# Optimization experiments

Measured on AMD Instinct MI355X. Metric: run time of the kernel, lower is better.

## Reference

```python
import jax, jax.numpy as jnp
import numpy as np


def setup_inputs() -> dict:
    key = jax.random.key(0)
    ks = jax.random.split(key, 16)
    B, T, A, R, M, D = 128, 1024, 512, 1024, 256, 256  # batch, max_time, annot, rnn, memory, attn dims
    F, K = 32, 31  # location filters, kernel size
    s = jnp.float32(0.02)
    return dict(
        memory=jax.random.normal(ks[0], (B, M), jnp.float32),
        context=jax.random.normal(ks[1], (B, A), jnp.float32),
        rnn_state=jax.random.normal(ks[2], (B, R), jnp.float32),
        annots=jax.random.normal(ks[3], (B, T, A), jnp.float32),
        atten=jax.random.uniform(ks[4], (B, 2, T), jnp.float32),
        mask=jax.random.randint(ks[5], (B, T), 0, 2).astype(jnp.int32),
        Wi=jax.random.normal(ks[6], (3 * R, A + M), jnp.float32) * s,   # GRU input weights (r,z,n)
        Wh=jax.random.normal(ks[7], (3 * R, R), jnp.float32) * s,       # GRU hidden weights
        bi=jnp.zeros((3 * R,), jnp.float32),
        bh=jnp.zeros((3 * R,), jnp.float32),
        conv_w=jax.random.normal(ks[8], (F, 2, K), jnp.float32) * s,    # loc_conv (OIH)
        loc_w=jax.random.normal(ks[9], (D, F), jnp.float32) * s,
        loc_b=jnp.zeros((D,), jnp.float32),
        q_w=jax.random.normal(ks[10], (D, R), jnp.float32) * s,
        q_b=jnp.zeros((D,), jnp.float32),
        a_w=jax.random.normal(ks[11], (D, A), jnp.float32) * s,
        a_b=jnp.zeros((D,), jnp.float32),
        v_w=jax.random.normal(ks[12], (1, D), jnp.float32) * s,
    )


def reference(memory, context, rnn_state, annots, atten, mask,
              Wi, Wh, bi, bh, conv_w, loc_w, loc_b, q_w, q_b, a_w, a_b, v_w):
    # --- GRUCell (torch gate order: r, z, n) ---
    x = jnp.concatenate([memory, context], axis=-1)          # (B, M+A)
    gi = x @ Wi.T + bi                                        # (B, 3R)
    gh = rnn_state @ Wh.T + bh                                # (B, 3R)
    ir, iz, inn = jnp.split(gi, 3, axis=-1)
    hr, hz, hn = jnp.split(gh, 3, axis=-1)
    r = jax.nn.sigmoid(ir + hr)
    z = jax.nn.sigmoid(iz + hz)
    n = jnp.tanh(inn + r * hn)
    h = (1.0 - z) * n + z * rnn_state                         # (B, R) rnn_output

    # --- Location-sensitive attention ---
    pad = (conv_w.shape[-1] - 1) // 2
    loc = jax.lax.conv_general_dilated(atten, conv_w, (1,), [(pad, pad)],
                                       dimension_numbers=('NCH', 'OIH', 'NCH'))  # (B, F, T)
    ploc = jnp.einsum('bft,df->btd', loc, loc_w) + loc_b      # (B, T, D)
    pq = (h @ q_w.T + q_b)[:, None, :]                        # (B, 1, D)
    pa = jnp.einsum('bta,da->btd', annots, a_w) + a_b         # (B, T, D)
    align = jnp.einsum('btd,d->bt', jnp.tanh(pq + pa + ploc), v_w[0])  # (B, T)

    # masked softmax (mask==0 -> -inf)
    align = jnp.where(mask != 0, align, jnp.float32(-1e30))
    align = jax.nn.softmax(align, axis=-1)

    # context = bmm(align, annots)
    ctx = jnp.einsum('bt,bta->ba', align, annots)             # (B, A)
    return (h, ctx, align)
```

## Files before the change

kernel.cpp:

```cpp
#include <hip/hip_runtime.h>
#include <cstddef>

constexpr int B  = 128;
constexpr int T  = 1024;
constexpr int AD = 512;
constexpr int R  = 1024;
constexpr int M  = 256;
constexpr int DD = 256;
constexpr int F  = 32;
constexpr int KW = 31;
constexpr int PADW = 15;
constexpr int XDIM = M + AD;
constexpr int G3 = 3 * R;
constexpr size_t BG3 = (size_t)B * G3;

using short8 = __attribute__((ext_vector_type(8))) short;
using f32x4  = __attribute__((ext_vector_type(4))) float;

__device__ __forceinline__ float sigmoidf(float x) { return 1.f / (1.f + __expf(-x)); }

__device__ __forceinline__ unsigned short f2bf(float x) {
  unsigned int u = __float_as_uint(x);
  u += 0x7FFFu + ((u >> 16) & 1u);
  return (unsigned short)(u >> 16);
}

__device__ __forceinline__ float tanh_fast(float x) {
  float e = __expf(2.f * x);
  return 1.f - 2.f / (e + 1.f);
}

__device__ __forceinline__ void load_lds16(const void* g, void* l) {
  __builtin_amdgcn_global_load_lds(
      (const __attribute__((address_space(1))) unsigned int*)g,
      (__attribute__((address_space(3))) unsigned int*)l, 16, 0, 0);
}

__global__ __launch_bounds__(256) void prep_wsw(const float* __restrict__ aw,
                                                const float* __restrict__ lw,
                                                unsigned short* __restrict__ awsw,
                                                unsigned short* __restrict__ lwsw) {
  int idx = blockIdx.x * 256 + threadIdx.x;
  int chunk = idx >> 10;
  int rn = (idx & 1023) >> 2;
  int u = idx & 3;
  int su = u ^ ((rn >> 1) & 3);
  const float* src;
  unsigned short* dst;
  if (chunk < 16) {
    src = aw + (size_t)rn * AD + chunk * 32 + u * 8;
    dst = awsw + chunk * 8192 + rn * 32 + su * 8;
  } else {
    src = lw + (size_t)rn * F + u * 8;
    dst = lwsw + rn * 32 + su * 8;
  }
  float4 f0 = *(const float4*)src;
  float4 f1 = *(const float4*)(src + 4);
  unsigned int w0 = f2bf(f0.x) | ((unsigned)f2bf(f0.y) << 16);
  unsigned int w1 = f2bf(f0.z) | ((unsigned)f2bf(f0.w) << 16);
  unsigned int w2 = f2bf(f1.x) | ((unsigned)f2bf(f1.y) << 16);
  unsigned int w3 = f2bf(f1.z) | ((unsigned)f2bf(f1.w) << 16);
  uint4 pk = {w0, w1, w2, w3};
  *(uint4*)dst = pk;
}

__global__ __launch_bounds__(256) void loc_conv(const float* __restrict__ atten,
                                                const float* __restrict__ conv_w,
                                                unsigned short* __restrict__ locw) {
  __shared__ float s_att[2 * 94];
  __shared__ float s_cw[F * 62];
  const int tid = threadIdx.x;
  const int t0 = blockIdx.x * 64, b = blockIdx.y;
  for (int i = tid; i < 2 * 94; i += 256) {
    int c = i / 94, ii = i - c * 94;
    int gt = t0 - PADW + ii;
    s_att[i] = (gt >= 0 && gt < T) ? atten[((size_t)b * 2 + c) * T + gt] : 0.f;
  }
  for (int i = tid; i < F * 62; i += 256) s_cw[i] = conv_w[i];
  __syncthreads();
  const int f = tid & 31;
  const int tb = (tid >> 5) * 8;
  float a8[8] = {0.f, 0.f, 0.f, 0.f, 0.f, 0.f, 0.f, 0.f};
#pragma unroll
  for (int c = 0; c < 2; ++c) {
    float win[38];
#pragma unroll
    for (int i = 0; i < 38; ++i) win[i] = s_att[c * 94 + tb + i];
#pragma unroll
    for (int k = 0; k < KW; ++k) {
      float w = s_cw[f * 62 + c * 31 + k];
#pragma unroll
      for (int ti = 0; ti < 8; ++ti) a8[ti] += w * win[ti + k];
    }
  }
#pragma unroll
  for (int ti = 0; ti < 8; ++ti)
    locw[((size_t)b * T + t0 + tb + ti) * F + f] = f2bf(a8[ti]);
}

__global__ __launch_bounds__(256) void gemm_fused8(const float* __restrict__ mem,
                                                   const float* __restrict__ ctxin,
                                                   const float* __restrict__ rnn,
                                                   const float* __restrict__ Wi,
                                                   const float* __restrict__ Wh,
                                                   float* __restrict__ outp) {
  __shared__ __align__(16) float sX[16 * 68];
  __shared__ __align__(16) float sW[16 * 68];
  const int z = blockIdx.z;
  const int which = z >> 2, q = z & 3;
  const float* __restrict__ W = which ? Wh : Wi;
  const int K = which ? R : XDIM;
  const int Kq = K >> 2;
  const int kbeg = q * Kq, kend = kbeg + Kq;
  float* __restrict__ C = outp + (size_t)z * BG3;
  const int tid = threadIdx.x;
  const int g0 = blockIdx.x * 64, b0 = blockIdx.y * 64;
  const int bg = tid & 15, gg = tid >> 4;
  const int lr = tid >> 2, c4 = (tid & 3) * 4;
  float acc[4][4] = {};
  for (int k0 = kbeg; k0 < kend; k0 += 16) {
    const int k = k0 + c4;
    float4 xv;
    if (which) xv = *(const float4*)&rnn[(size_t)(b0 + lr) * R + k];
    else if (k < M) xv = *(const float4*)&mem[(size_t)(b0 + lr) * M + k];
    else xv = *(const float4*)&ctxin[(size_t)(b0 + lr) * AD + (k - M)];
    float4 wv = *(const float4*)&W[(size_t)(g0 + lr) * K + k];
    sX[(c4 + 0) * 68 + lr] = xv.x; sX[(c4 + 1) * 68 + lr] = xv.y;
    sX[(c4 + 2) * 68 + lr] = xv.z; sX[(c4 + 3) * 68 + lr] = xv.w;
    sW[(c4 + 0) * 68 + lr] = wv.x; sW[(c4 + 1) * 68 + lr] = wv.y;
    sW[(c4 + 2) * 68 + lr] = wv.z; sW[(c4 + 3) * 68 + lr] = wv.w;
    __syncthreads();
#pragma unroll
    for (int k2 = 0; k2 < 16; ++k2) {
      float4 xr = *(const float4*)&sX[k2 * 68 + bg * 4];
      float4 wr = *(const float4*)&sW[k2 * 68 + gg * 4];
      float xa[4] = {xr.x, xr.y, xr.z, xr.w};
      float wa[4] = {wr.x, wr.y, wr.z, wr.w};
#pragma unroll
      for (int ib = 0; ib < 4; ++ib)
#pragma unroll
        for (int jg = 0; jg < 4; ++jg) acc[ib][jg] += xa[ib] * wa[jg];
    }
    __syncthreads();
  }
#pragma unroll
  for (int ib = 0; ib < 4; ++ib) {
    float4 o;
    o.x = acc[ib][0]; o.y = acc[ib][1]; o.z = acc[ib][2]; o.w = acc[ib][3];
    *(float4*)&C[(size_t)(b0 + bg * 4 + ib) * G3 + g0 + gg * 4] = o;
  }
}

__global__ __launch_bounds__(256) void gru_combine(const float* __restrict__ gp,
                                                   const float* __restrict__ bi,
                                                   const float* __restrict__ bh,
                                                   const float* __restrict__ hprev,
                                                   float* __restrict__ hout) {
  int idx = blockIdx.x * 256 + threadIdx.x;
  int b = idx >> 10, j = idx & (R - 1);
  float ir = bi[j], iz = bi[R + j], inn = bi[2 * R + j];
  float hr = bh[j], hz = bh[R + j], hn = bh[2 * R + j];
#pragma unroll
  for (int z = 0; z < 4; ++z) {
    const float* g = gp + (size_t)z * BG3 + (size_t)b * G3;
    ir += g[j]; iz += g[R + j]; inn += g[2 * R + j];
  }
#pragma unroll
  for (int z = 4; z < 8; ++z) {
    const float* g = gp + (size_t)z * BG3 + (size_t)b * G3;
    hr += g[j]; hz += g[R + j]; hn += g[2 * R + j];
  }
  float r = sigmoidf(ir + hr);
  float z = sigmoidf(iz + hz);
  float n = tanhf(inn + r * hn);
  float hp = hprev[(size_t)b * R + j];
  hout[(size_t)b * R + j] = (1.f - z) * n + z * hp;
}

__global__ __launch_bounds__(256) void pq_kernel(const float* __restrict__ h,
                                                 const float* __restrict__ q_w,
                                                 const float* __restrict__ q_b,
                                                 float* __restrict__ pq) {
  __shared__ __align__(16) float sh[R];
  int b = blockIdx.x, tid = threadIdx.x;
  ((float4*)sh)[tid] = ((const float4*)(h + (size_t)b * R))[tid];
  __syncthreads();
  const float* wr = q_w + (size_t)tid * R;
  float acc = 0.f;
#pragma unroll 4
  for (int k = 0; k < R; k += 4) {
    float4 w = *(const float4*)&wr[k];
    float4 x = *(const float4*)&sh[k];
    acc += w.x * x.x + w.y * x.y + w.z * x.z + w.w * x.w;
  }
  pq[(size_t)b * DD + tid] = acc + q_b[tid];
}

__global__ __launch_bounds__(512, 4) void attn_fused(
    const float* __restrict__ annots, const unsigned short* __restrict__ locw,
    const int* __restrict__ mask,
    const unsigned short* __restrict__ awsw, const unsigned short* __restrict__ lwsw,
    const float* __restrict__ loc_b, const float* __restrict__ a_b,
    const float* __restrict__ v_w, const float* __restrict__ pq,
    float* __restrict__ u_out, float* __restrict__ ctx_part,
    float* __restrict__ S_part) {
  __shared__ __align__(16) unsigned short s_A[2][128 * 32];
  __shared__ __align__(16) unsigned short s_B[2][256 * 32];

  const int tid = threadIdx.x;
  const int wv = tid >> 6, lane = tid & 63;
  const int lm = lane & 15, lg = lane >> 4;
  const int wr = wv >> 2, wc = wv & 3;
  const int g = blockIdx.x, b = blockIdx.y;
  const int t0 = g * 128;
  const int ar = tid >> 2, au = tid & 3;
  const int asu = au ^ ((ar >> 1) & 3);
  const int sufb = lg ^ ((lm >> 1) & 3);

  const float* arow = annots + ((size_t)b * T + t0 + ar) * AD + au * 8;

  {
    float4 f0 = *(const float4*)(arow);
    float4 f1 = *(const float4*)(arow + 4);
    load_lds16(awsw + wv * 1024 + lane * 8, &s_B[0][wv * 1024]);
    load_lds16(awsw + wv * 1024 + 512 + lane * 8, &s_B[0][wv * 1024 + 512]);
    unsigned int w0 = f2bf(f0.x) | ((unsigned)f2bf(f0.y) << 16);
    unsigned int w1 = f2bf(f0.z) | ((unsigned)f2bf(f0.w) << 16);
    unsigned int w2 = f2bf(f1.x) | ((unsigned)f2bf(f1.y) << 16);
    unsigned int w3 = f2bf(f1.z) | ((unsigned)f2bf(f1.w) << 16);
    uint4 pk = {w0, w1, w2, w3};
    *(uint4*)&s_A[0][ar * 32 + asu * 8] = pk;
  }
  float4 aN0 = *(const float4*)(arow + 32);
  float4 aN1 = *(const float4*)(arow + 36);
  uint4 lvN = {0, 0, 0, 0};

  f32x4 acc[4][4];
#pragma unroll
  for (int j = 0; j < 4; ++j) {
    int d = wc * 64 + j * 16 + lm;
    float base = pq[(size_t)b * DD + d] + a_b[d] + loc_b[d];
    f32x4 bv = {base, base, base, base};
#pragma unroll
    for (int i = 0; i < 4; ++i) acc[i][j] = bv;
  }
  __syncthreads();

#pragma unroll 1
  for (int ks = 0; ks <= 16; ++ks) {
    const int cur = ks & 1, nxt = cur ^ 1;
    if (ks + 1 <= 16) {
      const unsigned short* img = (ks + 1 < 16) ? (awsw + (ks + 1) * 8192) : lwsw;
      load_lds16(img + wv * 1024 + lane * 8, &s_B[nxt][wv * 1024]);
      load_lds16(img + wv * 1024 + 512 + lane * 8, &s_B[nxt][wv * 1024 + 512]);
    }
    float4 aN20, aN21;
    uint4 lvN2;
    if (ks + 2 <= 15) {
      aN20 = *(const float4*)(arow + (ks + 2) * 32);
      aN21 = *(const float4*)(arow + (ks + 2) * 32 + 4);
    } else if (ks + 2 == 16) {
      lvN2 = *(const uint4*)(locw + ((size_t)b * T + t0 + ar) * F + au * 8);
    }
    if (ks + 1 <= 15) {
      unsigned int w0 = f2bf(aN0.x) | ((unsigned)f2bf(aN0.y) << 16);
      unsigned int w1 = f2bf(aN0.z) | ((unsigned)f2bf(aN0.w) << 16);
      unsigned int w2 = f2bf(aN1.x) | ((unsigned)f2bf(aN1.y) << 16);
      unsigned int w3 = f2bf(aN1.z) | ((unsigned)f2bf(aN1.w) << 16);
      uint4 pk = {w0, w1, w2, w3};
      *(uint4*)&s_A[nxt][ar * 32 + asu * 8] = pk;
    } else if (ks + 1 == 16) {
      *(uint4*)&s_A[nxt][ar * 32 + asu * 8] = lvN;
    }
    short8 afr[4], bfr[4];
#pragma unroll
    for (int i = 0; i < 4; ++i)
      afr[i] = *(const short8*)&s_A[cur][(wr * 64 + i * 16 + lm) * 32 + sufb * 8];
#pragma unroll
    for (int j = 0; j < 4; ++j)
      bfr[j] = *(const short8*)&s_B[cur][(wc * 64 + j * 16 + lm) * 32 + sufb * 8];
#pragma unroll
    for (int j = 0; j < 4; ++j)
#pragma unroll
      for (int i = 0; i < 4; ++i)
        acc[i][j] = __builtin_amdgcn_mfma_f32_16x16x32_bf16(afr[i], bfr[j], acc[i][j], 0, 0, 0);
    if (ks <= 13) {
      asm volatile("s_waitcnt vmcnt(2) lgkmcnt(0)" ::: "memory");
    } else if (ks == 14) {
      asm volatile("s_waitcnt vmcnt(1) lgkmcnt(0)" ::: "memory");
    } else {
      asm volatile("s_waitcnt vmcnt(0) lgkmcnt(0)" ::: "memory");
    }
    __builtin_amdgcn_s_barrier();
    if (ks + 2 <= 15) { aN0 = aN20; aN1 = aN21; }
    else if (ks + 2 == 16) lvN = lvN2;
  }

  float* s_e = (float*)s_A;
  float* s_u = s_e + 512;
  float* s_red = s_e + 644;
  float vwv[4];
#pragma unroll
  for (int j = 0; j < 4; ++j) vwv[j] = v_w[wc * 64 + j * 16 + lm];
#pragma unroll
  for (int i = 0; i < 4; ++i) {
#pragma unroll
    for (int reg = 0; reg < 4; ++reg) {
      float p = 0.f;
#pragma unroll
      for (int j = 0; j < 4; ++j) p += vwv[j] * tanh_fast(acc[i][j][reg]);
      p += __shfl_xor(p, 1);
      p += __shfl_xor(p, 2);
      p += __shfl_xor(p, 4);
      p += __shfl_xor(p, 8);
      if (lm == 0) s_e[wc * 128 + wr * 64 + i * 16 + lg * 4 + reg] = p;
    }
  }
  __syncthreads();
  if (tid < 128) {
    float e = s_e[tid] + s_e[128 + tid] + s_e[256 + tid] + s_e[384 + tid];
    bool mk = mask[(size_t)b * T + t0 + tid] != 0;
    float u = mk ? __expf(e) : 0.f;
    u_out[(size_t)b * T + t0 + tid] = u;
    s_u[tid] = u;
    float p = u;
    p += __shfl_xor(p, 1);
    p += __shfl_xor(p, 2);
    p += __shfl_xor(p, 4);
    p += __shfl_xor(p, 8);
    p += __shfl_xor(p, 16);
    p += __shfl_xor(p, 32);
    if (lane == 0) s_red[tid >> 6] = p;
  }
  __syncthreads();
  if (tid == 0) S_part[b * 8 + g] = s_red[0] + s_red[1];
  {
    const float* ap = annots + ((size_t)b * T + t0) * AD + tid;
    float c0 = 0.f, c1 = 0.f, c2 = 0.f, c3 = 0.f;
#pragma unroll 2
    for (int t = 0; t < 128; t += 4) {
      c0 += s_u[t + 0] * ap[(size_t)(t + 0) * AD];
      c1 += s_u[t + 1] * ap[(size_t)(t + 1) * AD];
      c2 += s_u[t + 2] * ap[(size_t)(t + 2) * AD];
      c3 += s_u[t + 3] * ap[(size_t)(t + 3) * AD];
    }
    ctx_part[(size_t)g * ((size_t)B * AD) + (size_t)b * AD + tid] = (c0 + c1) + (c2 + c3);
  }
}

__global__ __launch_bounds__(512) void finalize(const float* __restrict__ S_part,
                                                const float* __restrict__ ctx_part,
                                                float* __restrict__ al,
                                                float* __restrict__ ctxo) {
  int b = blockIdx.x, tid = threadIdx.x;
  float S = 0.f;
#pragma unroll
  for (int g = 0; g < 8; ++g) S += S_part[b * 8 + g];
  float inv = 1.f / S;
  float2* ap = (float2*)(al + (size_t)b * T);
  float2 v = ap[tid];
  v.x *= inv; v.y *= inv;
  ap[tid] = v;
  float c = 0.f;
#pragma unroll
  for (int p = 0; p < 8; ++p)
    c += ctx_part[(size_t)p * ((size_t)B * AD) + (size_t)b * AD + tid];
  ctxo[(size_t)b * AD + tid] = c * inv;
}

extern "C" void kernel_launch(void* const* d_in, const int* in_sizes, int n_in,
                              void* d_out, int out_size, void* d_ws, size_t ws_size,
                              hipStream_t stream) {
  const float* memory = (const float*)d_in[0];
  const float* context = (const float*)d_in[1];
  const float* rnn = (const float*)d_in[2];
  const float* annots = (const float*)d_in[3];
  const float* atten = (const float*)d_in[4];
  const int* mask = (const int*)d_in[5];
  const float* Wi = (const float*)d_in[6];
  const float* Wh = (const float*)d_in[7];
  const float* bi = (const float*)d_in[8];
  const float* bh = (const float*)d_in[9];
  const float* conv_w = (const float*)d_in[10];
  const float* loc_w = (const float*)d_in[11];
  const float* loc_b = (const float*)d_in[12];
  const float* q_w = (const float*)d_in[13];
  const float* q_b = (const float*)d_in[14];
  const float* a_w = (const float*)d_in[15];
  const float* a_b = (const float*)d_in[16];
  const float* v_w = (const float*)d_in[17];

  float* out = (float*)d_out;
  float* out_h = out;
  float* out_ctx = out + (size_t)B * R;
  float* out_al = out_ctx + (size_t)B * AD;

  float* ws = (float*)d_ws;
  float* gp_ws = ws;
  float* pq_ws = gp_ws + 8 * BG3;
  float* S_part = pq_ws + (size_t)B * DD;
  float* ctx_part = S_part + (size_t)B * 8;
  unsigned short* awsw = (unsigned short*)(ctx_part + (size_t)8 * B * AD);
  unsigned short* lwsw = awsw + (size_t)16 * 8192;
  unsigned short* locws = lwsw + 8192;

  prep_wsw<<<68, 256, 0, stream>>>(a_w, loc_w, awsw, lwsw);
  loc_conv<<<dim3(T / 64, B), 256, 0, stream>>>(atten, conv_w, locws);
  gemm_fused8<<<dim3(G3 / 64, B / 64, 8), 256, 0, stream>>>(memory, context, rnn,
                                                            Wi, Wh, gp_ws);
  gru_combine<<<(B * R) / 256, 256, 0, stream>>>(gp_ws, bi, bh, rnn, out_h);
  pq_kernel<<<B, 256, 0, stream>>>(out_h, q_w, q_b, pq_ws);
  attn_fused<<<dim3(8, B), 512, 0, stream>>>(annots, locws, mask, awsw, lwsw,
                                             loc_b, a_b, v_w, pq_ws,
                                             out_al, ctx_part, S_part);
  finalize<<<B, 512, 0, stream>>>(S_part, ctx_part, out_al, out_ctx);
}
```

Before: 190.2 us.

## Convert GRU GEMM inputs to bf16 and compute gates with MFMA

Adds a prep kernel that converts Wi, Wh, the concatenated input and the hidden state to bf16 in workspace. The fp32 LDS-tiled FMA GEMM is replaced by an MFMA 16x16x32 bf16 kernel that reads fragments straight from global memory, with no LDS staging, still split-K into 8 partials. The aim is to swap slow scalar FP32 FMAs for matrix cores. In exchange it adds a full pass over the weights every call (fp32 read plus bf16 write), uses bf16 precision for the GRU, and the direct global fragment loads are not coalesced.

```diff
diff --git a/kernel.cpp b/kernel.cpp
--- a/kernel.cpp
+++ b/kernel.cpp
@@ -28,6 +28,15 @@
 __device__ __forceinline__ float tanh_fast(float x) {
   float e = __expf(2.f * x);
   return 1.f - 2.f / (e + 1.f);
+}
+
+__device__ __forceinline__ uint4 pack_bf8(float4 f0, float4 f1) {
+  uint4 r;
+  r.x = f2bf(f0.x) | ((unsigned)f2bf(f0.y) << 16);
+  r.y = f2bf(f0.z) | ((unsigned)f2bf(f0.w) << 16);
+  r.z = f2bf(f1.x) | ((unsigned)f2bf(f1.y) << 16);
+  r.w = f2bf(f1.z) | ((unsigned)f2bf(f1.w) << 16);
+  return r;
 }
 
 __device__ __forceinline__ void load_lds16(const void* g, void* l) {
@@ -56,12 +65,42 @@
   }
   float4 f0 = *(const float4*)src;
   float4 f1 = *(const float4*)(src + 4);
-  unsigned int w0 = f2bf(f0.x) | ((unsigned)f2bf(f0.y) << 16);
-  unsigned int w1 = f2bf(f0.z) | ((unsigned)f2bf(f0.w) << 16);
-  unsigned int w2 = f2bf(f1.x) | ((unsigned)f2bf(f1.y) << 16);
-  unsigned int w3 = f2bf(f1.z) | ((unsigned)f2bf(f1.w) << 16);
-  uint4 pk = {w0, w1, w2, w3};
-  *(uint4*)dst = pk;
+  *(uint4*)dst = pack_bf8(f0, f1);
+}
+
+__global__ __launch_bounds__(256) void prep_gru(const float* __restrict__ mem,
+                                                const float* __restrict__ ctxin,
+                                                const float* __restrict__ rnn,
+                                                const float* __restrict__ Wi,
+                                                const float* __restrict__ Wh,
+                                                unsigned short* __restrict__ Wib,
+                                                unsigned short* __restrict__ Whb,
+                                                unsigned short* __restrict__ xb,
+                                                unsigned short* __restrict__ rnnb) {
+  const int t = blockIdx.x * 256 + threadIdx.x;
+  const float* src;
+  unsigned short* dst;
+  if (t < 294912) {
+    src = Wi + (size_t)t * 8;
+    dst = Wib + (size_t)t * 8;
+  } else if (t < 688128) {
+    size_t e = (size_t)(t - 294912) * 8;
+    src = Wh + e;
+    dst = Whb + e;
+  } else if (t < 700416) {
+    size_t e = (size_t)(t - 688128) * 8;
+    int row = (int)(e / XDIM), col = (int)(e % XDIM);
+    src = (col < M) ? (mem + (size_t)row * M + col)
+                    : (ctxin + (size_t)row * AD + (col - M));
+    dst = xb + e;
+  } else {
+    size_t e = (size_t)(t - 700416) * 8;
+    src = rnn + e;
+    dst = rnnb + e;
+  }
+  float4 f0 = *(const float4*)src;
+  float4 f1 = *(const float4*)(src + 4);
+  *(uint4*)dst = pack_bf8(f0, f1);
 }
 
 __global__ __launch_bounds__(256) void loc_conv(const float* __restrict__ atten,
@@ -98,57 +137,58 @@
     locw[((size_t)b * T + t0 + tb + ti) * F + f] = f2bf(a8[ti]);
 }
 
-__global__ __launch_bounds__(256) void gemm_fused8(const float* __restrict__ mem,
-                                                   const float* __restrict__ ctxin,
-                                                   const float* __restrict__ rnn,
-                                                   const float* __restrict__ Wi,
-                                                   const float* __restrict__ Wh,
+__global__ __launch_bounds__(256, 2) void gemm_gru(const unsigned short* __restrict__ xb,
+                                                   const unsigned short* __restrict__ rnnb,
+                                                   const unsigned short* __restrict__ Wib,
+                                                   const unsigned short* __restrict__ Whb,
                                                    float* __restrict__ outp) {
-  __shared__ __align__(16) float sX[16 * 68];
-  __shared__ __align__(16) float sW[16 * 68];
-  const int z = blockIdx.z;
+  const int tid = threadIdx.x;
+  const int wv = tid >> 6, lane = tid & 63;
+  const int lm = lane & 15, lg = lane >> 4;
+  const int g0 = blockIdx.x * 64;
+  const int z = blockIdx.y;
   const int which = z >> 2, q = z & 3;
-  const float* __restrict__ W = which ? Wh : Wi;
+  const unsigned short* __restrict__ A = which ? rnnb : xb;
+  const unsigned short* __restrict__ W = which ? Whb : Wib;
   const int K = which ? R : XDIM;
   const int Kq = K >> 2;
-  const int kbeg = q * Kq, kend = kbeg + Kq;
+  const int nch = Kq >> 5;
   float* __restrict__ C = outp + (size_t)z * BG3;
-  const int tid = threadIdx.x;
-  const int g0 = blockIdx.x * 64, b0 = blockIdx.y * 64;
-  const int bg = tid & 15, gg = tid >> 4;
-  const int lr = tid >> 2, c4 = (tid & 3) * 4;
-  float acc[4][4] = {};
-  for (int k0 = kbeg; k0 < kend; k0 += 16) {
-    const int k = k0 + c4;
-    float4 xv;
-    if (which) xv = *(const float4*)&rnn[(size_t)(b0 + lr) * R + k];
-    else if (k < M) xv = *(const float4*)&mem[(size_t)(b0 + lr) * M + k];
-    else xv = *(const float4*)&ctxin[(size_t)(b0 + lr) * AD + (k - M)];
-    float4 wv = *(const float4*)&W[(size_t)(g0 + lr) * K + k];
-    sX[(c4 + 0) * 68 + lr] = xv.x; sX[(c4 + 1) * 68 + lr] = xv.y;
-    sX[(c4 + 2) * 68 + lr] = xv.z; sX[(c4 + 3) * 68 + lr] = xv.w;
-    sW[(c4 + 0) * 68 + lr] = wv.x; sW[(c4 + 1) * 68 + lr] = wv.y;
-    sW[(c4 + 2) * 68 + lr] = wv.z; sW[(c4 + 3) * 68 + lr] = wv.w;
-    __syncthreads();
-#pragma unroll
-    for (int k2 = 0; k2 < 16; ++k2) {
-      float4 xr = *(const float4*)&sX[k2 * 68 + bg * 4];
-      float4 wr = *(const float4*)&sW[k2 * 68 + gg * 4];
-      float xa[4] = {xr.x, xr.y, xr.z, xr.w};
-      float wa[4] = {wr.x, wr.y, wr.z, wr.w};
-#pragma unroll
-      for (int ib = 0; ib < 4; ++ib)
-#pragma unroll
-        for (int jg = 0; jg < 4; ++jg) acc[ib][jg] += xa[ib] * wa[jg];
-    }
-    __syncthreads();
-  }
-#pragma unroll
-  for (int ib = 0; ib < 4; ++ib) {
-    float4 o;
-    o.x = acc[ib][0]; o.y = acc[ib][1]; o.z = acc[ib][2]; o.w = acc[ib][3];
-    *(float4*)&C[(size_t)(b0 + bg * 4 + ib) * G3 + g0 + gg * 4] = o;
-  }
+
+  const unsigned short* aA = A + (size_t)(wv * 32 + lm) * K + q * Kq + lg * 8;
+  const unsigned short* bW = W + (size_t)(g0 + lm) * K + q * Kq + lg * 8;
+
+  f32x4 acc[2][4];
+#pragma unroll
+  for (int i = 0; i < 2; ++i)
+#pragma unroll
+    for (int j = 0; j < 4; ++j) acc[i][j] = (f32x4){0.f, 0.f, 0.f, 0.f};
+
+#pragma unroll 2
+  for (int ch = 0; ch < nch; ++ch) {
+    const int k = ch * 32;
+    short8 a8[2], b8[4];
+#pragma unroll
+    for (int i = 0; i < 2; ++i)
+      a8[i] = *(const short8*)(aA + (size_t)i * 16 * K + k);
+#pragma unroll
+    for (int j = 0; j < 4; ++j)
+      b8[j] = *(const short8*)(bW + (size_t)j * 16 * K + k);
+#pragma unroll
+    for (int j = 0; j < 4; ++j)
+#pragma unroll
+      for (int i = 0; i < 2; ++i)
+        acc[i][j] = __builtin_amdgcn_mfma_f32_16x16x32_bf16(a8[i], b8[j], acc[i][j], 0, 0, 0);
+  }
+
+#pragma unroll
+  for (int i = 0; i < 2; ++i)
+#pragma unroll
+    for (int reg = 0; reg < 4; ++reg) {
+      const size_t row = (size_t)(wv * 32 + i * 16 + lg * 4 + reg) * G3 + g0 + lm;
+#pragma unroll
+      for (int j = 0; j < 4; ++j) C[row + j * 16] = acc[i][j][reg];
+    }
 }
 
 __global__ __launch_bounds__(256) void gru_combine(const float* __restrict__ gp,
@@ -224,12 +264,7 @@
     float4 f1 = *(const float4*)(arow + 4);
     load_lds16(awsw + wv * 1024 + lane * 8, &s_B[0][wv * 1024]);
     load_lds16(awsw + wv * 1024 + 512 + lane * 8, &s_B[0][wv * 1024 + 512]);
-    unsigned int w0 = f2bf(f0.x) | ((unsigned)f2bf(f0.y) << 16);
-    unsigned int w1 = f2bf(f0.z) | ((unsigned)f2bf(f0.w) << 16);
-    unsigned int w2 = f2bf(f1.x) | ((unsigned)f2bf(f1.y) << 16);
-    unsigned int w3 = f2bf(f1.z) | ((unsigned)f2bf(f1.w) << 16);
-    uint4 pk = {w0, w1, w2, w3};
-    *(uint4*)&s_A[0][ar * 32 + asu * 8] = pk;
+    *(uint4*)&s_A[0][ar * 32 + asu * 8] = pack_bf8(f0, f1);
   }
   float4 aN0 = *(const float4*)(arow + 32);
   float4 aN1 = *(const float4*)(arow + 36);
@@ -263,12 +298,7 @@
       lvN2 = *(const uint4*)(locw + ((size_t)b * T + t0 + ar) * F + au * 8);
     }
     if (ks + 1 <= 15) {
-      unsigned int w0 = f2bf(aN0.x) | ((unsigned)f2bf(aN0.y) << 16);
-      unsigned int w1 = f2bf(aN0.z) | ((unsigned)f2bf(aN0.w) << 16);
-      unsigned int w2 = f2bf(aN1.x) | ((unsigned)f2bf(aN1.y) << 16);
-      unsigned int w3 = f2bf(aN1.z) | ((unsigned)f2bf(aN1.w) << 16);
-      uint4 pk = {w0, w1, w2, w3};
-      *(uint4*)&s_A[nxt][ar * 32 + asu * 8] = pk;
+      *(uint4*)&s_A[nxt][ar * 32 + asu * 8] = pack_bf8(aN0, aN1);
     } else if (ks + 1 == 16) {
       *(uint4*)&s_A[nxt][ar * 32 + asu * 8] = lvN;
     }
@@ -402,15 +432,20 @@
   float* ctx_part = S_part + (size_t)B * 8;
   unsigned short* awsw = (unsigned short*)(ctx_part + (size_t)8 * B * AD);
   unsigned short* lwsw = awsw + (size_t)16 * 8192;
-  unsigned short* locws = lwsw + 8192;
+  unsigned short* locw = lwsw + 8192;
+  unsigned short* Wib = locw + (size_t)B * T * F;
+  unsigned short* Whb = Wib + (size_t)G3 * XDIM;
+  unsigned short* xb = Whb + (size_t)G3 * R;
+  unsigned short* rnnb = xb + (size_t)B * XDIM;
 
   prep_wsw<<<68, 256, 0, stream>>>(a_w, loc_w, awsw, lwsw);
-  loc_conv<<<dim3(T / 64, B), 256, 0, stream>>>(atten, conv_w, locws);
-  gemm_fused8<<<dim3(G3 / 64, B / 64, 8), 256, 0, stream>>>(memory, context, rnn,
-                                                            Wi, Wh, gp_ws);
+  prep_gru<<<2800, 256, 0, stream>>>(memory, context, rnn, Wi, Wh,
+                                     Wib, Whb, xb, rnnb);
+  loc_conv<<<dim3(T / 64, B), 256, 0, stream>>>(atten, conv_w, locw);
+  gemm_gru<<<dim3(48, 8), 256, 0, stream>>>(xb, rnnb, Wib, Whb, gp_ws);
   gru_combine<<<(B * R) / 256, 256, 0, stream>>>(gp_ws, bi, bh, rnn, out_h);
   pq_kernel<<<B, 256, 0, stream>>>(out_h, q_w, q_b, pq_ws);
-  attn_fused<<<dim3(8, B), 512, 0, stream>>>(annots, locws, mask, awsw, lwsw,
+  attn_fused<<<dim3(8, B), 512, 0, stream>>>(annots, locw, mask, awsw, lwsw,
                                              loc_b, a_b, v_w, pq_ws,
                                              out_al, ctx_part, S_part);
   finalize<<<B, 512, 0, stream>>>(S_part, ctx_part, out_al, out_ctx);
```

After: 185.0 us. 2.7% less time.
